# Performance work log

Hardware: AMD Instinct MI355X
Metric: run time of the kernel (lower is better)

Reference implementation:

```python
import jax, jax.numpy as jnp
import numpy as np

TAU = 1.0

def setup_inputs() -> dict:
    key = jax.random.key(0)
    k1, k2, k3 = jax.random.split(key, 3)
    B, D, C = 16384, 1024, 1000
    hidden_states = jax.random.normal(k1, (B, D), dtype=jnp.float32)
    prototype_matrix = jax.random.normal(k2, (C, D), dtype=jnp.float32)
    labels = jax.random.randint(k3, (B,), 0, C, dtype=jnp.int64)
    return {"hidden_states": hidden_states, "prototype_matrix": prototype_matrix, "labels": labels}

def reference(hidden_states, prototype_matrix, labels):
    # Per-sample L2 normalize (matches x / x.norm())
    x = hidden_states / jnp.linalg.norm(hidden_states, axis=-1, keepdims=True)  # [B, D]
    # Cosine-similarity logits against class prototypes, scaled by tau=1.0
    logits = jnp.einsum('bd,cd->bc', x, prototype_matrix) / TAU  # [B, C]
    # -log( exp(logit_y) / sum exp(logits) ) == cross-entropy with log_softmax
    logp = jax.nn.log_softmax(logits, axis=-1)
    per_loss = -jnp.take_along_axis(logp, labels[:, None], axis=1)[:, 0]  # [B]
    return jnp.mean(per_loss)  # reduction='mean'
```

## Files before the change

kernel.cpp:

```cpp
#include <hip/hip_runtime.h>
#include <hip/hip_bf16.h>

#define B_ROWS 16384
#define DDIM   1024
#define CCLS   1000
#define CPAD   1024
#define GN     4
#define NKT    16

typedef __attribute__((ext_vector_type(8))) short  short8;
typedef __attribute__((ext_vector_type(4))) float  f32x4;

static __device__ __forceinline__ unsigned short f2bf(float f) {
    unsigned int u = __float_as_uint(f);
    unsigned int r = 0x7fffu + ((u >> 16) & 1u);
    return (unsigned short)((u + r) >> 16);
}

static __device__ __forceinline__ void gl_lds16(const unsigned short* g, unsigned short* l) {
    __builtin_amdgcn_global_load_lds(
        (const __attribute__((address_space(1))) void*)g,
        (__attribute__((address_space(3))) void*)l, 16, 0, 0);
}

__global__ __launch_bounds__(256) void prep(
        const float* __restrict__ H, const float* __restrict__ P,
        unsigned short* __restrict__ Hb, unsigned short* __restrict__ Pb,
        float* __restrict__ rowscale) {
    const int bid = blockIdx.x;
    const int tid = threadIdx.x;
    const int w   = tid >> 6;
    const int l   = tid & 63;
    if (bid < 2048) {
        #pragma unroll
        for (int p = 0; p < 2; ++p) {
            const int row = bid * 8 + w * 2 + p;
            const float* src = H + (size_t)row * DDIM;
            unsigned short* dst = Hb + (size_t)row * DDIM;
            float ss = 0.f;
            #pragma unroll
            for (int c = 0; c < 4; ++c) {
                const int col = c * 256 + l * 4;
                const float4 v = *reinterpret_cast<const float4*>(src + col);
                ss += v.x*v.x + v.y*v.y + v.z*v.z + v.w*v.w;
                ushort4 o = {f2bf(v.x), f2bf(v.y), f2bf(v.z), f2bf(v.w)};
                *reinterpret_cast<ushort4*>(dst + col) = o;
            }
            #pragma unroll
            for (int mask = 1; mask < 64; mask <<= 1)
                ss += __shfl_xor(ss, mask);
            if (l == 0) rowscale[row] = 1.4426950408889634f * rsqrtf(ss);
        }
    } else {
        const int pb = bid - 2048;
        #pragma unroll 4
        for (int c = 0; c < 32; ++c) {
            const int base = (pb * 8192 + c * 256 + tid) * 4;
            const int row  = base >> 10;
            ushort4 o;
            if (row < CCLS) {
                const float4 v = *reinterpret_cast<const float4*>(P + base);
                o.x = f2bf(v.x); o.y = f2bf(v.y); o.z = f2bf(v.z); o.w = f2bf(v.w);
            } else {
                o.x = o.y = o.z = o.w = 0;
            }
            *reinterpret_cast<ushort4*>(Pb + base) = o;
        }
    }
}

__global__ __launch_bounds__(512, 2) void gemm_ce(
        const unsigned short* __restrict__ Hb,
        const unsigned short* __restrict__ Pb,
        const int* __restrict__ labels,
        const float* __restrict__ rowscale,
        float* __restrict__ psum,
        float* __restrict__ plab) {
    __shared__ unsigned short Alds[2][256 * 64];
    __shared__ unsigned short Blds[2][256 * 64];

    const int orig = blockIdx.x;
    const int wg   = (orig & 7) * 32 + (orig >> 3);
    const int bm   = wg >> 2;
    const int bn   = wg & 3;

    const int tid = threadIdx.x;
    const int w   = tid >> 6;
    const int l   = tid & 63;
    const int lo  = l & 15;
    const int hi  = l >> 4;
    const int wm  = w >> 2;
    const int wn  = w & 3;

    const size_t arow0 = (size_t)bm * 256;
    const size_t brow0 = (size_t)bn * 256;

    const int srow = l >> 3;
    const int scol = ((l & 7) ^ srow) * 8;

#define STAGE_A(buf_, t_, q_) gl_lds16(                                         \
        Hb + (arow0 + (q_) * 64 + w * 8 + srow) * DDIM + (t_) * 64 + scol,      \
        &Alds[buf_][((q_) * 64 + w * 8) * 64])
#define STAGE_B(buf_, t_, q_) gl_lds16(                                         \
        Pb + (brow0 + (q_) * 64 + w * 8 + srow) * DDIM + (t_) * 64 + scol,      \
        &Blds[buf_][((q_) * 64 + w * 8) * 64])

    f32x4 acc[8][4];
    #pragma unroll
    for (int m = 0; m < 8; ++m)
        #pragma unroll
        for (int n = 0; n < 4; ++n)
            acc[m][n] = (f32x4){0.f, 0.f, 0.f, 0.f};

    const int swz   = (lo & 7) << 4;
    const int colk0 = (hi << 4) ^ swz;
    const int colk1 = (64 | (hi << 4)) ^ swz;

    short8 a[4][2];
    short8 b[4][2];

#define LDA(base_, mh_) do { _Pragma("unroll")                                  \
    for (int mi_ = 0; mi_ < 4; ++mi_) {                                         \
        const int r_ = (wm * 128 + (mh_) * 64 + mi_ * 16 + lo) * 128;           \
        a[mi_][0] = *reinterpret_cast<const short8*>((base_) + r_ + colk0);     \
        a[mi_][1] = *reinterpret_cast<const short8*>((base_) + r_ + colk1);     \
    } } while (0)
#define LDB(base_, nh_) do { _Pragma("unroll")                                  \
    for (int ni_ = 0; ni_ < 2; ++ni_) {                                         \
        const int r_ = (wn * 64 + ((nh_) * 2 + ni_) * 16 + lo) * 128;           \
        b[(nh_)*2+ni_][0] = *reinterpret_cast<const short8*>((base_) + r_ + colk0); \
        b[(nh_)*2+ni_][1] = *reinterpret_cast<const short8*>((base_) + r_ + colk1); \
    } } while (0)
#define MFMA_Q(mh_, nh_) do { _Pragma("unroll")                                 \
    for (int kk_ = 0; kk_ < 2; ++kk_) { _Pragma("unroll")                       \
    for (int ni_ = 0; ni_ < 2; ++ni_) { _Pragma("unroll")                       \
    for (int mi_ = 0; mi_ < 4; ++mi_) {                                         \
        acc[(mh_)*4+mi_][(nh_)*2+ni_] = __builtin_amdgcn_mfma_f32_16x16x32_bf16(\
            a[mi_][kk_], b[(nh_)*2+ni_][kk_], acc[(mh_)*4+mi_][(nh_)*2+ni_],    \
            0, 0, 0);                                                           \
    } } } } while (0)
#define PHASE_TAIL(mh_, nh_)                                                    \
    __builtin_amdgcn_s_barrier();                                               \
    asm volatile("s_waitcnt lgkmcnt(0)" ::: "memory");                          \
    __builtin_amdgcn_sched_barrier(0);                                          \
    __builtin_amdgcn_s_setprio(1);                                              \
    MFMA_Q(mh_, nh_);                                                           \
    __builtin_amdgcn_s_setprio(0);                                              \
    __builtin_amdgcn_s_barrier()

#define TILE_ITER(p_, t_) do {                                                  \
    const char* Ab_ = (const char*)&Alds[p_][0];                                \
    const char* Bb_ = (const char*)&Blds[p_][0];                                \
                                                                   \
    LDA(Ab_, 0); LDB(Bb_, 0);                                                   \
    if ((t_) + 1 < NKT) { STAGE_A((p_) ^ 1, (t_) + 1, 1);                       \
                          STAGE_A((p_) ^ 1, (t_) + 1, 3); }                     \
    PHASE_TAIL(0, 0);                                                           \
                                                                   \
    LDB(Bb_, 1);                                                                \
    if ((t_) + 2 < NKT) { STAGE_A(p_, (t_) + 2, 0); STAGE_A(p_, (t_) + 2, 2); } \
    PHASE_TAIL(0, 1);                                                           \
                                                                   \
    LDA(Ab_, 1);                                                                \
    if ((t_) + 2 < NKT) { STAGE_B(p_, (t_) + 2, 0); STAGE_B(p_, (t_) + 2, 1); } \
    PHASE_TAIL(1, 0);                                                           \
                                                                   \
    if ((t_) + 2 < NKT) { STAGE_B(p_, (t_) + 2, 2); STAGE_B(p_, (t_) + 2, 3);   \
        asm volatile("s_waitcnt vmcnt(6)" ::: "memory");                        \
    } else if ((t_) + 1 < NKT) {                                                \
        asm volatile("s_waitcnt vmcnt(0)" ::: "memory");                        \
    }                                                                           \
    PHASE_TAIL(1, 1);                                                           \
} while (0)

    #pragma unroll
    for (int q = 0; q < 4; ++q) { STAGE_A(0, 0, q); STAGE_B(0, 0, q); }
    STAGE_A(1, 1, 0); STAGE_A(1, 1, 2);
    #pragma unroll
    for (int q = 0; q < 4; ++q) STAGE_B(1, 1, q);
    asm volatile("s_waitcnt vmcnt(6)" ::: "memory");
    __builtin_amdgcn_s_barrier();

    #pragma unroll 1
    for (int kt2 = 0; kt2 < NKT / 2; ++kt2) {
        const int t0 = 2 * kt2;
        TILE_ITER(0, t0);
        TILE_ITER(1, t0 + 1);
    }
#undef TILE_ITER
#undef PHASE_TAIL
#undef MFMA_Q
#undef LDB
#undef LDA
#undef STAGE_B
#undef STAGE_A

    float* red = reinterpret_cast<float*>(&Alds[0][0]);
    #pragma unroll
    for (int m = 0; m < 8; ++m) {
        const int rloc = wm * 128 + m * 16 + hi * 4;
        float rs4[4], s4[4], lb2[4];
        int   lb4[4];
        #pragma unroll
        for (int j = 0; j < 4; ++j) {
            const size_t grow = arow0 + rloc + j;
            rs4[j] = rowscale[grow];
            lb4[j] = labels[grow];
            s4[j]  = 0.f;
            lb2[j] = -1e30f;
        }
        #pragma unroll
        for (int n = 0; n < 4; ++n) {
            const int c = (int)brow0 + wn * 64 + n * 16 + lo;
            const float pen = (c < CCLS) ? 0.f : -1e30f;
            #pragma unroll
            for (int j = 0; j < 4; ++j) {
                const float lg = fmaf(acc[m][n][j], rs4[j], pen);
                lb2[j] = (c == lb4[j]) ? lg : lb2[j];
                s4[j] += exp2f(lg);
            }
        }
        #pragma unroll
        for (int j = 0; j < 4; ++j) {
            #pragma unroll
            for (int mask = 1; mask <= 8; mask <<= 1) {
                s4[j]  += __shfl_xor(s4[j], mask);
                lb2[j]  = fmaxf(lb2[j], __shfl_xor(lb2[j], mask));
            }
            if (lo == 0) {
                const int r = rloc + j;
                red[(r * 4 + wn) * 2 + 0] = s4[j];
                red[(r * 4 + wn) * 2 + 1] = lb2[j];
            }
        }
    }
    __syncthreads();
    if (tid < 256) {
        float st = 0.f, lt = -1e30f;
        #pragma unroll
        for (int q = 0; q < 4; ++q) {
            st += red[(tid * 4 + q) * 2 + 0];
            lt  = fmaxf(lt, red[(tid * 4 + q) * 2 + 1]);
        }
        const size_t grow = arow0 + tid;
        psum[grow * GN + bn] = st;
        plab[grow * GN + bn] = lt;
    }
}

__global__ __launch_bounds__(1024) void reduce_all(
        const float* __restrict__ psum, const float* __restrict__ plab,
        float* __restrict__ out) {
    const int tid = threadIdx.x;
    float loss = 0.f;
    #pragma unroll 4
    for (int i = 0; i < B_ROWS / 1024; ++i) {
        const int row = i * 1024 + tid;
        const float4 ps = *reinterpret_cast<const float4*>(psum + (size_t)row * GN);
        const float4 pl = *reinterpret_cast<const float4*>(plab + (size_t)row * GN);
        const float st = (ps.x + ps.y) + (ps.z + ps.w);
        const float lt = fmaxf(fmaxf(pl.x, pl.y), fmaxf(pl.z, pl.w));
        loss += 0.6931471805599453f * (log2f(st) - lt);
    }
    #pragma unroll
    for (int mask = 1; mask < 64; mask <<= 1)
        loss += __shfl_xor(loss, mask);
    __shared__ float wsum[16];
    if ((tid & 63) == 0) wsum[tid >> 6] = loss;
    __syncthreads();
    if (tid < 64) {
        float v = (tid < 16) ? wsum[tid] : 0.f;
        #pragma unroll
        for (int mask = 1; mask < 16; mask <<= 1)
            v += __shfl_xor(v, mask);
        if (tid == 0) out[0] = v * (1.0f / 16384.0f);
    }
}

extern "C" void kernel_launch(void* const* d_in, const int* in_sizes, int n_in,
                              void* d_out, int out_size, void* d_ws, size_t ws_size,
                              hipStream_t stream) {
    const float* H      = (const float*)d_in[0];
    const float* P      = (const float*)d_in[1];
    const int*   labels = (const int*)d_in[2];
    float* out = (float*)d_out;

    char* wp = (char*)d_ws;
    unsigned short* Hb = (unsigned short*)wp;   wp += (size_t)B_ROWS * DDIM * 2;
    unsigned short* Pb = (unsigned short*)wp;   wp += (size_t)CPAD * DDIM * 2;
    float* rowscale    = (float*)wp;            wp += (size_t)B_ROWS * 4;
    float* psum        = (float*)wp;            wp += (size_t)B_ROWS * GN * 4;
    float* plab        = (float*)wp;

    prep<<<2080, 256, 0, stream>>>(H, P, Hb, Pb, rowscale);
    gemm_ce<<<(B_ROWS / 256) * GN, 512, 0, stream>>>(Hb, Pb, labels, rowscale, psum, plab);
    reduce_all<<<1, 1024, 0, stream>>>(psum, plab, out);
}
```

Before: 74.09 us.

## Overlap LDS fragment loads with MFMA phases and batch prep row loads

The GEMM main loop is reorganised so that LDS reads of A/B fragments for the next phase (and the next k-tile's first fragments) are issued during or right after the current MFMA block. This drops the explicit lgkmcnt(0) waits and sched_barriers and relies on compiler-inserted waits plus memory fences around barriers. The aim is to hide LDS latency behind MFMA work. Separately, the prep kernel now has each wave process 4 rows with all 16 float4 loads issued up front, halving the block count to raise memory-level parallelism. The GEMM change risks extra register pressure and a less precise wait schedule.

```diff
diff --git a/kernel.cpp b/kernel.cpp
--- a/kernel.cpp
+++ b/kernel.cpp
@@ -10,6 +10,8 @@
 
 typedef __attribute__((ext_vector_type(8))) short  short8;
 typedef __attribute__((ext_vector_type(4))) float  f32x4;
+
+#define FENCE asm volatile("" ::: "memory")
 
 static __device__ __forceinline__ unsigned short f2bf(float f) {
     unsigned int u = __float_as_uint(f);
@@ -31,36 +33,48 @@
     const int tid = threadIdx.x;
     const int w   = tid >> 6;
     const int l   = tid & 63;
-    if (bid < 2048) {
-        #pragma unroll
-        for (int p = 0; p < 2; ++p) {
-            const int row = bid * 8 + w * 2 + p;
-            const float* src = H + (size_t)row * DDIM;
-            unsigned short* dst = Hb + (size_t)row * DDIM;
-            float ss = 0.f;
+    if (bid < 1024) {
+        const int row0 = bid * 16 + w * 4;
+        float4 v[4][4];
+        #pragma unroll
+        for (int r = 0; r < 4; ++r)
+            #pragma unroll
+            for (int c = 0; c < 4; ++c)
+                v[r][c] = *reinterpret_cast<const float4*>(
+                    H + (size_t)(row0 + r) * DDIM + c * 256 + l * 4);
+        float ss[4];
+        #pragma unroll
+        for (int r = 0; r < 4; ++r) {
+            unsigned short* dst = Hb + (size_t)(row0 + r) * DDIM;
+            ss[r] = 0.f;
             #pragma unroll
             for (int c = 0; c < 4; ++c) {
-                const int col = c * 256 + l * 4;
-                const float4 v = *reinterpret_cast<const float4*>(src + col);
-                ss += v.x*v.x + v.y*v.y + v.z*v.z + v.w*v.w;
-                ushort4 o = {f2bf(v.x), f2bf(v.y), f2bf(v.z), f2bf(v.w)};
-                *reinterpret_cast<ushort4*>(dst + col) = o;
-            }
-            #pragma unroll
-            for (int mask = 1; mask < 64; mask <<= 1)
-                ss += __shfl_xor(ss, mask);
-            if (l == 0) rowscale[row] = 1.4426950408889634f * rsqrtf(ss);
+                const float4 q = v[r][c];
+                ss[r] += q.x*q.x + q.y*q.y + q.z*q.z + q.w*q.w;
+                ushort4 o = {f2bf(q.x), f2bf(q.y), f2bf(q.z), f2bf(q.w)};
+                *reinterpret_cast<ushort4*>(dst + c * 256 + l * 4) = o;
+            }
+        }
+        #pragma unroll
+        for (int mask = 1; mask < 64; mask <<= 1)
+            #pragma unroll
+            for (int r = 0; r < 4; ++r)
+                ss[r] += __shfl_xor(ss[r], mask);
+        if (l == 0) {
+            #pragma unroll
+            for (int r = 0; r < 4; ++r)
+                rowscale[row0 + r] = 1.4426950408889634f * rsqrtf(ss[r]);
         }
     } else {
-        const int pb = bid - 2048;
+        const int pb = bid - 1024;
         #pragma unroll 4
         for (int c = 0; c < 32; ++c) {
             const int base = (pb * 8192 + c * 256 + tid) * 4;
             const int row  = base >> 10;
             ushort4 o;
             if (row < CCLS) {
-                const float4 v = *reinterpret_cast<const float4*>(P + base);
-                o.x = f2bf(v.x); o.y = f2bf(v.y); o.z = f2bf(v.z); o.w = f2bf(v.w);
+                const float4 q = *reinterpret_cast<const float4*>(P + base);
+                o.x = f2bf(q.x); o.y = f2bf(q.y); o.z = f2bf(q.z); o.w = f2bf(q.w);
             } else {
                 o.x = o.y = o.z = o.w = 0;
             }
@@ -113,64 +127,71 @@
             acc[m][n] = (f32x4){0.f, 0.f, 0.f, 0.f};
 
     const int swz   = (lo & 7) << 4;
-    const int colk0 = (hi << 4) ^ swz;
-    const int colk1 = (64 | (hi << 4)) ^ swz;
+    const int colk[2] = { (hi << 4) ^ swz, (64 | (hi << 4)) ^ swz };
 
     short8 a[4][2];
     short8 b[4][2];
 
-#define LDA(base_, mh_) do { _Pragma("unroll")                                  \
+#define LDA_KK(buf_, mh_, kk_) do { _Pragma("unroll")                           \
     for (int mi_ = 0; mi_ < 4; ++mi_) {                                         \
         const int r_ = (wm * 128 + (mh_) * 64 + mi_ * 16 + lo) * 128;           \
-        a[mi_][0] = *reinterpret_cast<const short8*>((base_) + r_ + colk0);     \
-        a[mi_][1] = *reinterpret_cast<const short8*>((base_) + r_ + colk1);     \
+        a[mi_][kk_] = *reinterpret_cast<const short8*>(                         \
+            (const char*)&Alds[buf_][0] + r_ + colk[kk_]);                      \
     } } while (0)
-#define LDB(base_, nh_) do { _Pragma("unroll")                                  \
+#define LDB_(buf_, nh_) do { _Pragma("unroll")                                  \
     for (int ni_ = 0; ni_ < 2; ++ni_) {                                         \
         const int r_ = (wn * 64 + ((nh_) * 2 + ni_) * 16 + lo) * 128;           \
-        b[(nh_)*2+ni_][0] = *reinterpret_cast<const short8*>((base_) + r_ + colk0); \
-        b[(nh_)*2+ni_][1] = *reinterpret_cast<const short8*>((base_) + r_ + colk1); \
+        b[(nh_)*2+ni_][0] = *reinterpret_cast<const short8*>(                   \
+            (const char*)&Blds[buf_][0] + r_ + colk[0]);                        \
+        b[(nh_)*2+ni_][1] = *reinterpret_cast<const short8*>(                   \
+            (const char*)&Blds[buf_][0] + r_ + colk[1]);                        \
     } } while (0)
-#define MFMA_Q(mh_, nh_) do { _Pragma("unroll")                                 \
+#define MFMA_Q(mh_, nh_) do {                                                   \
+    __builtin_amdgcn_s_setprio(1);                                              \
+    _Pragma("unroll")                                                           \
     for (int kk_ = 0; kk_ < 2; ++kk_) { _Pragma("unroll")                       \
     for (int ni_ = 0; ni_ < 2; ++ni_) { _Pragma("unroll")                       \
     for (int mi_ = 0; mi_ < 4; ++mi_) {                                         \
         acc[(mh_)*4+mi_][(nh_)*2+ni_] = __builtin_amdgcn_mfma_f32_16x16x32_bf16(\
             a[mi_][kk_], b[(nh_)*2+ni_][kk_], acc[(mh_)*4+mi_][(nh_)*2+ni_],    \
             0, 0, 0);                                                           \
-    } } } } while (0)
-#define PHASE_TAIL(mh_, nh_)                                                    \
-    __builtin_amdgcn_s_barrier();                                               \
-    asm volatile("s_waitcnt lgkmcnt(0)" ::: "memory");                          \
-    __builtin_amdgcn_sched_barrier(0);                                          \
-    __builtin_amdgcn_s_setprio(1);                                              \
-    MFMA_Q(mh_, nh_);                                                           \
+    } } }                                                                       \
     __builtin_amdgcn_s_setprio(0);                                              \
-    __builtin_amdgcn_s_barrier()
+} while (0)
+#define BAR do { FENCE; __builtin_amdgcn_s_barrier(); FENCE; } while (0)
 
 #define TILE_ITER(p_, t_) do {                                                  \
-    const char* Ab_ = (const char*)&Alds[p_][0];                                \
-    const char* Bb_ = (const char*)&Blds[p_][0];                                \
-                                                                   \
-    LDA(Ab_, 0); LDB(Bb_, 0);                                                   \
+                                                   \
+    LDB_(p_, 1);                                              \
     if ((t_) + 1 < NKT) { STAGE_A((p_) ^ 1, (t_) + 1, 1);                       \
                           STAGE_A((p_) ^ 1, (t_) + 1, 3); }                     \
-    PHASE_TAIL(0, 0);                                                           \
-                                                                   \
-    LDB(Bb_, 1);                                                                \
+    BAR;                                                                        \
+    MFMA_Q(0, 0);                                                               \
+    BAR;                                                                        \
+                                                   \
     if ((t_) + 2 < NKT) { STAGE_A(p_, (t_) + 2, 0); STAGE_A(p_, (t_) + 2, 2); } \
-    PHASE_TAIL(0, 1);                                                           \
-                                                                   \
-    LDA(Ab_, 1);                                                                \
+    BAR;                                                                        \
+    MFMA_Q(0, 1);                                                               \
+    LDA_KK(p_, 1, 0);                                     \
+    BAR;                                                                        \
+                                                   \
+    LDA_KK(p_, 1, 1);                                               \
     if ((t_) + 2 < NKT) { STAGE_B(p_, (t_) + 2, 0); STAGE_B(p_, (t_) + 2, 1); } \
-    PHASE_TAIL(1, 0);                                                           \
-                                                                   \
+    BAR;                                                                        \
+    MFMA_Q(1, 0);                                                               \
+    BAR;                                                                        \
+                                                   \
     if ((t_) + 2 < NKT) { STAGE_B(p_, (t_) + 2, 2); STAGE_B(p_, (t_) + 2, 3);   \
         asm volatile("s_waitcnt vmcnt(6)" ::: "memory");                        \
     } else if ((t_) + 1 < NKT) {                                                \
         asm volatile("s_waitcnt vmcnt(0)" ::: "memory");                        \
     }                                                                           \
-    PHASE_TAIL(1, 1);                                                           \
+    BAR;                                                                        \
+    MFMA_Q(1, 1);                                                               \
+    if ((t_) + 1 < NKT) {                                 \
+        LDA_KK((p_) ^ 1, 0, 0); LDA_KK((p_) ^ 1, 0, 1); LDB_((p_) ^ 1, 0);      \
+    }                                                                           \
+    BAR;                                                                        \
 } while (0)
 
     #pragma unroll
@@ -179,7 +200,8 @@
     #pragma unroll
     for (int q = 0; q < 4; ++q) STAGE_B(1, 1, q);
     asm volatile("s_waitcnt vmcnt(6)" ::: "memory");
-    __builtin_amdgcn_s_barrier();
+    BAR;
+    LDA_KK(0, 0, 0); LDA_KK(0, 0, 1); LDB_(0, 0);
 
     #pragma unroll 1
     for (int kt2 = 0; kt2 < NKT / 2; ++kt2) {
@@ -188,10 +210,10 @@
         TILE_ITER(1, t0 + 1);
     }
 #undef TILE_ITER
-#undef PHASE_TAIL
+#undef BAR
 #undef MFMA_Q
-#undef LDB
-#undef LDA
+#undef LDB_
+#undef LDA_KK
 #undef STAGE_B
 #undef STAGE_A
 
@@ -292,7 +314,7 @@
     float* psum        = (float*)wp;            wp += (size_t)B_ROWS * GN * 4;
     float* plab        = (float*)wp;
 
-    prep<<<2080, 256, 0, stream>>>(H, P, Hb, Pb, rowscale);
+    prep<<<1056, 256, 0, stream>>>(H, P, Hb, Pb, rowscale);
     gemm_ce<<<(B_ROWS / 256) * GN, 512, 0, stream>>>(Hb, Pb, labels, rowscale, psum, plab);
     reduce_all<<<1, 1024, 0, stream>>>(psum, plab, out);
 }
```

Measured after the change: 78.89 us (median of 2 runs). 1.06x slower.

## Batch four rows per wave in prep and split final reduction across blocks

Applied to the files above, without the earlier changes.

The prep kernel now has each wave load four H rows (16 float4 loads issued up front) before converting and reducing, which halves the grid and raises memory-level parallelism. The single-block final reduction is replaced by a 64-block partial reduction plus a tiny second kernel, spreading the psum/plab reads across the GPU. The cost is an extra kernel launch and more registers per thread in prep.

```diff
diff --git a/kernel.cpp b/kernel.cpp
--- a/kernel.cpp
+++ b/kernel.cpp
@@ -31,36 +31,48 @@
     const int tid = threadIdx.x;
     const int w   = tid >> 6;
     const int l   = tid & 63;
-    if (bid < 2048) {
-        #pragma unroll
-        for (int p = 0; p < 2; ++p) {
-            const int row = bid * 8 + w * 2 + p;
-            const float* src = H + (size_t)row * DDIM;
-            unsigned short* dst = Hb + (size_t)row * DDIM;
-            float ss = 0.f;
+    if (bid < 1024) {
+        const int row0 = bid * 16 + w * 4;
+        float4 v[4][4];
+        #pragma unroll
+        for (int r = 0; r < 4; ++r)
+            #pragma unroll
+            for (int c = 0; c < 4; ++c)
+                v[r][c] = *reinterpret_cast<const float4*>(
+                    H + (size_t)(row0 + r) * DDIM + c * 256 + l * 4);
+        float ss[4];
+        #pragma unroll
+        for (int r = 0; r < 4; ++r) {
+            unsigned short* dst = Hb + (size_t)(row0 + r) * DDIM;
+            ss[r] = 0.f;
             #pragma unroll
             for (int c = 0; c < 4; ++c) {
-                const int col = c * 256 + l * 4;
-                const float4 v = *reinterpret_cast<const float4*>(src + col);
-                ss += v.x*v.x + v.y*v.y + v.z*v.z + v.w*v.w;
-                ushort4 o = {f2bf(v.x), f2bf(v.y), f2bf(v.z), f2bf(v.w)};
-                *reinterpret_cast<ushort4*>(dst + col) = o;
-            }
-            #pragma unroll
-            for (int mask = 1; mask < 64; mask <<= 1)
-                ss += __shfl_xor(ss, mask);
-            if (l == 0) rowscale[row] = 1.4426950408889634f * rsqrtf(ss);
+                const float4 q = v[r][c];
+                ss[r] += q.x*q.x + q.y*q.y + q.z*q.z + q.w*q.w;
+                ushort4 o = {f2bf(q.x), f2bf(q.y), f2bf(q.z), f2bf(q.w)};
+                *reinterpret_cast<ushort4*>(dst + c * 256 + l * 4) = o;
+            }
+        }
+        #pragma unroll
+        for (int mask = 1; mask < 64; mask <<= 1)
+            #pragma unroll
+            for (int r = 0; r < 4; ++r)
+                ss[r] += __shfl_xor(ss[r], mask);
+        if (l == 0) {
+            #pragma unroll
+            for (int r = 0; r < 4; ++r)
+                rowscale[row0 + r] = 1.4426950408889634f * rsqrtf(ss[r]);
         }
     } else {
-        const int pb = bid - 2048;
+        const int pb = bid - 1024;
         #pragma unroll 4
         for (int c = 0; c < 32; ++c) {
             const int base = (pb * 8192 + c * 256 + tid) * 4;
             const int row  = base >> 10;
             ushort4 o;
             if (row < CCLS) {
-                const float4 v = *reinterpret_cast<const float4*>(P + base);
-                o.x = f2bf(v.x); o.y = f2bf(v.y); o.z = f2bf(v.z); o.w = f2bf(v.w);
+                const float4 q = *reinterpret_cast<const float4*>(P + base);
+                o.x = f2bf(q.x); o.y = f2bf(q.y); o.z = f2bf(q.z); o.w = f2bf(q.w);
             } else {
                 o.x = o.y = o.z = o.w = 0;
             }
@@ -248,33 +260,32 @@
     }
 }
 
-__global__ __launch_bounds__(1024) void reduce_all(
+__global__ __launch_bounds__(256) void reduce1(
         const float* __restrict__ psum, const float* __restrict__ plab,
-        float* __restrict__ out) {
+        float* __restrict__ partials) {
     const int tid = threadIdx.x;
-    float loss = 0.f;
-    #pragma unroll 4
-    for (int i = 0; i < B_ROWS / 1024; ++i) {
-        const int row = i * 1024 + tid;
-        const float4 ps = *reinterpret_cast<const float4*>(psum + (size_t)row * GN);
-        const float4 pl = *reinterpret_cast<const float4*>(plab + (size_t)row * GN);
-        const float st = (ps.x + ps.y) + (ps.z + ps.w);
-        const float lt = fmaxf(fmaxf(pl.x, pl.y), fmaxf(pl.z, pl.w));
-        loss += 0.6931471805599453f * (log2f(st) - lt);
-    }
+    const size_t row = (size_t)blockIdx.x * 256 + tid;
+    const float4 ps = *reinterpret_cast<const float4*>(psum + row * GN);
+    const float4 pl = *reinterpret_cast<const float4*>(plab + row * GN);
+    const float st = (ps.x + ps.y) + (ps.z + ps.w);
+    const float lt = fmaxf(fmaxf(pl.x, pl.y), fmaxf(pl.z, pl.w));
+    float loss = 0.6931471805599453f * (log2f(st) - lt);
     #pragma unroll
     for (int mask = 1; mask < 64; mask <<= 1)
         loss += __shfl_xor(loss, mask);
-    __shared__ float wsum[16];
+    __shared__ float wsum[4];
     if ((tid & 63) == 0) wsum[tid >> 6] = loss;
     __syncthreads();
-    if (tid < 64) {
-        float v = (tid < 16) ? wsum[tid] : 0.f;
-        #pragma unroll
-        for (int mask = 1; mask < 16; mask <<= 1)
-            v += __shfl_xor(v, mask);
-        if (tid == 0) out[0] = v * (1.0f / 16384.0f);
-    }
+    if (tid == 0)
+        partials[blockIdx.x] = wsum[0] + wsum[1] + wsum[2] + wsum[3];
+}
+
+__global__ void reduce2(const float* __restrict__ partials, float* __restrict__ out) {
+    float v = partials[threadIdx.x];
+    #pragma unroll
+    for (int mask = 1; mask < 64; mask <<= 1)
+        v += __shfl_xor(v, mask);
+    if (threadIdx.x == 0) out[0] = v * (1.0f / 16384.0f);
 }
 
 extern "C" void kernel_launch(void* const* d_in, const int* in_sizes, int n_in,
@@ -290,9 +301,11 @@
     unsigned short* Pb = (unsigned short*)wp;   wp += (size_t)CPAD * DDIM * 2;
     float* rowscale    = (float*)wp;            wp += (size_t)B_ROWS * 4;
     float* psum        = (float*)wp;            wp += (size_t)B_ROWS * GN * 4;
-    float* plab        = (float*)wp;
-
-    prep<<<2080, 256, 0, stream>>>(H, P, Hb, Pb, rowscale);
+    float* plab        = (float*)wp;            wp += (size_t)B_ROWS * GN * 4;
+    float* partials    = (float*)wp;
+
+    prep<<<1056, 256, 0, stream>>>(H, P, Hb, Pb, rowscale);
     gemm_ce<<<(B_ROWS / 256) * GN, 512, 0, stream>>>(Hb, Pb, labels, rowscale, psum, plab);
-    reduce_all<<<1, 1024, 0, stream>>>(psum, plab, out);
-}
+    reduce1<<<B_ROWS / 256, 256, 0, stream>>>(psum, plab, partials);
+    reduce2<<<1, 64, 0, stream>>>(partials, out);
+}
```

After: 71.84 us. 3.0% less time.
